# Kernel optimization log

Measured on AMD Instinct MI355X. Metric: run time of the kernel, lower is better.

The kernel has to match this reference:

```python
import jax, jax.numpy as jnp
import numpy as np

B, N, F, O = 8, 4096, 512, 512
D = F // 8  # fc1/fc2 projection dim = 64


def setup_inputs() -> dict:
    key = jax.random.key(0)
    ks = jax.random.split(key, 8)
    x = jax.random.normal(ks[0], (B, N, F), dtype=jnp.float32)
    mask = jax.random.randint(ks[1], (B, N), 0, 2).astype(jnp.float32)
    s1 = 1.0 / np.sqrt(F)
    w1 = jax.random.uniform(ks[2], (F, D), jnp.float32, -s1, s1)
    b1 = jnp.zeros((D,), jnp.float32)
    w2 = jax.random.uniform(ks[3], (F, D), jnp.float32, -s1, s1)
    b2 = jnp.zeros((D,), jnp.float32)
    s2 = 1.0 / np.sqrt(O)
    weight = jax.random.uniform(ks[4], (F, O), jnp.float32, -s2, s2)
    return {"x": x, "mask": mask, "w1": w1, "b1": b1, "w2": w2, "b2": b2, "weight": weight}


def reference(x, mask, w1, b1, w2, b2, weight):
    # q, k: [B, N, D]
    q = x @ w1 + b1
    k = x @ w2 + b2
    scale = jnp.sqrt(jnp.asarray(D, x.dtype))
    # sim: [B, N, N]
    sim = jnp.einsum('bnd,bmd->bnm', q, k) / scale
    # NOTE: mask.unsqueeze(-1) -> [B, N, 1]: masks QUERY rows (faithful to source)
    neg = jnp.asarray(-1e12, x.dtype)
    sim = sim + (1.0 - mask)[:, :, None] * neg
    adj = jax.nn.softmax(sim, axis=-1) * mask[:, :, None]
    support = x @ weight  # [B, N, O]
    return jnp.einsum('bnm,bmo->bno', adj, support)
```

## Files before the change

kernel.cpp:

```cpp
#include <hip/hip_runtime.h>

constexpr int BB = 8, NN = 4096, FF = 512, DD = 64, OO = 512;

using short8  = __attribute__((ext_vector_type(8))) short;
using ushort8 = __attribute__((ext_vector_type(8))) unsigned short;
using ushort4v= __attribute__((ext_vector_type(4))) unsigned short;
using f32x4   = __attribute__((ext_vector_type(4))) float;

__device__ __forceinline__ unsigned short f2bf(float f) {
  unsigned int u = __builtin_bit_cast(unsigned int, f);
  return (unsigned short)((u + 0x7FFFu + ((u >> 16) & 1u)) >> 16);
}

__device__ __forceinline__ f32x4 mfma16(short8 a, short8 b, f32x4 c) {
  return __builtin_amdgcn_mfma_f32_16x16x32_bf16(a, b, c, 0, 0, 0);
}

__device__ __forceinline__ void gl_lds16(const void* g, void* s) {
  __builtin_amdgcn_global_load_lds(
      (const __attribute__((address_space(1))) unsigned int*)g,
      (__attribute__((address_space(3))) unsigned int*)s,
      16, 0, 0);
}

__global__ void cast_x(const float* __restrict__ x, unsigned short* __restrict__ xb) {
  size_t base = ((size_t)blockIdx.x * 256 + threadIdx.x) * 8;
  float4 a = *(const float4*)(x + base);
  float4 b = *(const float4*)(x + base + 4);
  ushort8 o;
  o[0]=f2bf(a.x); o[1]=f2bf(a.y); o[2]=f2bf(a.z); o[3]=f2bf(a.w);
  o[4]=f2bf(b.x); o[5]=f2bf(b.y); o[6]=f2bf(b.z); o[7]=f2bf(b.w);
  *(ushort8*)(xb + base) = o;
}

__global__ void build_w(const float* __restrict__ w1, const float* __restrict__ w2,
                        const float* __restrict__ wgt,
                        const float* __restrict__ b1, const float* __restrict__ b2,
                        unsigned short* __restrict__ Wt, float* __restrict__ bias) {
  int idx = blockIdx.x * 256 + threadIdx.x;
  int j = idx >> 9, kk = idx & 511;
  float v = (j < 64) ? w1[kk * 64 + j]
          : (j < 128) ? w2[kk * 64 + (j - 64)]
                      : wgt[(size_t)kk * 512 + (j - 128)];
  Wt[(size_t)j * 512 + kk] = f2bf(v);
  if (kk == 0) bias[j] = (j < 64) ? b1[j] : (j < 128) ? b2[j - 64] : 0.f;
}

__global__ void compact_rows(const float* __restrict__ mask, int* __restrict__ cnt,
                             int* __restrict__ ridx) {
  __shared__ int wsum[4];
  __shared__ int base;
  const int b = blockIdx.x;
  const int t = threadIdx.x, lane = t & 63, w = t >> 6;
  if (t == 0) base = 0;
  __syncthreads();
  for (int it = 0; it < 16; ++it) {
    int r = it * 256 + t;
    bool act = mask[(b << 12) + r] != 0.f;
    unsigned long long bal = __ballot(act);
    int pre = __popcll(bal & ((1ull << lane) - 1ull));
    if (lane == 0) wsum[w] = __popcll(bal);
    __syncthreads();
    int woff = 0;
    for (int i = 0; i < w; ++i) woff += wsum[i];
    int tot = wsum[0] + wsum[1] + wsum[2] + wsum[3];
    if (act) ridx[(b << 12) + base + woff + pre] = r;
    __syncthreads();
    if (t == 0) base += tot;
    __syncthreads();
  }
  if (t == 0) cnt[b] = base;
}

__global__ void zero_masked(const float* __restrict__ mask, float* __restrict__ out) {
  int gid = blockIdx.x * 256 + threadIdx.x;
  int r = gid >> 7, c = (gid & 127) * 4;
  if (mask[r] == 0.f) {
    float4 z = {0.f, 0.f, 0.f, 0.f};
    *(float4*)(out + (size_t)r * 512 + c) = z;
  }
}

__global__ __launch_bounds__(256, 2) void proj_gemm(
    const unsigned short* __restrict__ X, const unsigned short* __restrict__ Wt,
    const float* __restrict__ bias,
    unsigned short* __restrict__ QK, unsigned short* __restrict__ SupT) {
  __shared__ __align__(16) unsigned short Abuf[128 * 64];
  __shared__ __align__(16) unsigned short Bbuf[128 * 64];
  const int t = threadIdx.x, lane = t & 63, w = t >> 6;
  const int nblk = blockIdx.x;
  const int m0 = blockIdx.y * 128, n0 = nblk * 128;
  const int wm = w & 1, wn = w >> 1;

  f32x4 acc[4][4] = {};
  for (int kt = 0; kt < 8; ++kt) {
    for (int i = 0; i < 4; ++i) {
      int c = i * 4 + w;
      int row = c * 8 + (lane >> 3);
      int k0 = (lane & 7) * 8;
      gl_lds16(X + (size_t)(m0 + row) * 512 + kt * 64 + k0, &Abuf[c * 512]);
      gl_lds16(Wt + (size_t)(n0 + row) * 512 + kt * 64 + k0, &Bbuf[c * 512]);
    }
    __syncthreads();
    short8 af[4][2], bfr[4][2];
    for (int mi = 0; mi < 4; ++mi)
      for (int kc = 0; kc < 2; ++kc) {
        int row = wm * 64 + mi * 16 + (lane & 15);
        int d = kc * 32 + (lane >> 4) * 8;
        af[mi][kc] = *(const short8*)&Abuf[row * 64 + d];
      }
    for (int ni = 0; ni < 4; ++ni)
      for (int kc = 0; kc < 2; ++kc) {
        int col = wn * 64 + ni * 16 + (lane & 15);
        int d = kc * 32 + (lane >> 4) * 8;
        bfr[ni][kc] = *(const short8*)&Bbuf[col * 64 + d];
      }
    for (int mi = 0; mi < 4; ++mi)
      for (int ni = 0; ni < 4; ++ni)
        for (int kc = 0; kc < 2; ++kc)
          acc[mi][ni] = mfma16(af[mi][kc], bfr[ni][kc], acc[mi][ni]);
    __syncthreads();
  }
  for (int mi = 0; mi < 4; ++mi)
    for (int ni = 0; ni < 4; ++ni) {
      int col_g = n0 + wn * 64 + ni * 16 + (lane & 15);
      int row0 = m0 + wm * 64 + mi * 16 + ((lane >> 4) * 4);
      float bv = bias[col_g];
      if (nblk == 0) {
        for (int j = 0; j < 4; ++j)
          QK[(size_t)(row0 + j) * 128 + col_g] = f2bf(acc[mi][ni][j] + bv);
      } else {
        int scol = col_g - 128;
        int b = row0 >> 12, rl = row0 & 4095;
        ushort4v pk;
        for (int j = 0; j < 4; ++j) pk[j] = f2bf(acc[mi][ni][j] + bv);
        *(ushort4v*)&SupT[(size_t)(b * 512 + scol) * 4096 + rl] = pk;
      }
    }
}

__global__ __launch_bounds__(512, 6) void attn_kernel(
    const unsigned short* __restrict__ QK, const unsigned short* __restrict__ SupT,
    const int* __restrict__ cnt, const int* __restrict__ ridx,
    float* __restrict__ out) {
  __shared__ __align__(16) unsigned short Kb[2][32 * 64];
  __shared__ __align__(16) unsigned short Vt[2][256 * 32];
  __shared__ __align__(16) unsigned short Pb[2][64 * 40];
  __shared__ float lsh[2][64];
  __shared__ int rsh[64];

  const int batch = blockIdx.x & 7;
  const int rest  = blockIdx.x >> 3;
  const int chunk = rest >> 1, colh = rest & 1;
  const int n_act = cnt[batch];
  if (chunk * 64 >= n_act) return;
  const int rem = min(64, n_act - chunk * 64);

  const int t = threadIdx.x, lane = t & 63, w = t >> 6;
  const int keybase = batch << 12;
  const int wm = w >> 2;
  const int wq = w & 3;
  const int fms = wq >> 1, ks = wq & 1;
  const int wo = w & 3;

  if (t < 64) rsh[t] = ridx[(batch << 12) + chunk * 64 + min(t, rem - 1)];
  __syncthreads();

  short8 aq[2];
  {
    int rl = rsh[wm * 32 + fms * 16 + (lane & 15)];
    for (int kc = 0; kc < 2; ++kc)
      aq[kc] = *(const short8*)&QK[(size_t)(keybase + rl) * 128 + kc * 32 + (lane >> 4) * 8];
  }

  f32x4 acc[2][4] = {};
  float lacc[4] = {0.f, 0.f, 0.f, 0.f};
  const int rl0 = wm * 32 + fms * 16 + (lane >> 4) * 4;

  auto stage = [&](int p, int key0) {
    if (w < 4) {
      int key = w * 8 + (lane >> 3);
      int q = lane & 7;
      int d0 = (q ^ (key & 7)) * 8;
      gl_lds16(QK + (size_t)(keybase + key0 + key) * 128 + 64 + d0, &Kb[p][w * 512]);
    }
    for (int i = 0; i < 2; ++i) {
      int c = i * 8 + w;
      int colL = c * 16 + (lane >> 2);
      int q = lane & 3;
      int k0 = (q ^ ((colL >> 1) & 3)) * 8;
      gl_lds16(SupT + (size_t)(batch * 512 + colh * 256 + colL) * 4096 + key0 + k0,
               &Vt[p][c * 512]);
    }
  };

  stage(0, 0);
  for (int kt = 0; kt < 128; ++kt) {
    const int p = kt & 1;
    asm volatile("s_waitcnt vmcnt(0)" ::: "memory");
    asm volatile("s_barrier" ::: "memory");

    if (kt < 127) stage(p ^ 1, (kt + 1) * 32);

    {
      f32x4 sa = {0.f, 0.f, 0.f, 0.f};
      int key = ks * 16 + (lane & 15);
      __builtin_amdgcn_s_setprio(1);
      for (int kc = 0; kc < 2; ++kc) {
        int dblk = kc * 4 + (lane >> 4);
        int blk = dblk ^ (key & 7);
        short8 bk = *(const short8*)&Kb[p][key * 64 + blk * 8];
        sa = mfma16(aq[kc], bk, sa);
      }
      __builtin_amdgcn_s_setprio(0);
      for (int j = 0; j < 4; ++j) {
        float pv = __expf(sa[j] * 0.125f);
        lacc[j] += pv;
        Pb[p][(rl0 + j) * 40 + key] = f2bf(pv);
      }
    }
    asm volatile("s_waitcnt lgkmcnt(0)" ::: "memory");
    asm volatile("s_barrier" ::: "memory");

    short8 pa[2];
    for (int fm = 0; fm < 2; ++fm) {
      int row = wm * 32 + fm * 16 + (lane & 15);
      pa[fm] = *(const short8*)&Pb[p][row * 40 + (lane >> 4) * 8];
    }
    __builtin_amdgcn_s_setprio(1);
    for (int ni = 0; ni < 4; ++ni) {
      int colL = wo * 64 + ni * 16 + (lane & 15);
      int blk = (lane >> 4) ^ ((colL >> 1) & 3);
      short8 vb = *(const short8*)&Vt[p][colL * 32 + blk * 8];
      acc[0][ni] = mfma16(pa[0], vb, acc[0][ni]);
      acc[1][ni] = mfma16(pa[1], vb, acc[1][ni]);
    }
    __builtin_amdgcn_s_setprio(0);
  }

  for (int j = 0; j < 4; ++j) {
    float v = lacc[j];
    v += __shfl_xor(v, 1); v += __shfl_xor(v, 2);
    v += __shfl_xor(v, 4); v += __shfl_xor(v, 8);
    lacc[j] = v;
  }
  if ((lane & 15) == 0) {
    for (int j = 0; j < 4; ++j) lsh[ks][rl0 + j] = lacc[j];
  }
  __syncthreads();

  for (int fm = 0; fm < 2; ++fm)
    for (int ni = 0; ni < 4; ++ni) {
      int colL = wo * 64 + ni * 16 + (lane & 15);
      int sl0 = wm * 32 + fm * 16 + (lane >> 4) * 4;
      for (int j = 0; j < 4; ++j) {
        if (sl0 + j < rem) {
          float linv = 1.f / (lsh[0][sl0 + j] + lsh[1][sl0 + j]);
          int rl = rsh[sl0 + j];
          float av = ((float*)&acc[fm][ni])[j];
          out[(size_t)(keybase + rl) * 512 + colh * 256 + colL] = av * linv;
        }
      }
    }
}

extern "C" void kernel_launch(void* const* d_in, const int* in_sizes, int n_in,
                              void* d_out, int out_size, void* d_ws, size_t ws_size,
                              hipStream_t stream) {
  const float* x    = (const float*)d_in[0];
  const float* mask = (const float*)d_in[1];
  const float* w1   = (const float*)d_in[2];
  const float* b1   = (const float*)d_in[3];
  const float* w2   = (const float*)d_in[4];
  const float* b2   = (const float*)d_in[5];
  const float* wgt  = (const float*)d_in[6];
  float* out = (float*)d_out;

  char* ws = (char*)d_ws;
  unsigned short* Xb   = (unsigned short*)(ws);
  unsigned short* QK   = (unsigned short*)(ws + 33554432);
  unsigned short* SupT = (unsigned short*)(ws + 41943040);
  unsigned short* Wt   = (unsigned short*)(ws + 75497472);
  float* bias          = (float*)(ws + 76152832);
  int*   cnt           = (int*)(ws + 76417536);
  int*   ridx          = (int*)(ws + 76417664);

  build_w<<<dim3(1280), dim3(256), 0, stream>>>(w1, w2, wgt, b1, b2, Wt, bias);
  compact_rows<<<dim3(8), dim3(256), 0, stream>>>(mask, cnt, ridx);
  cast_x<<<dim3(8192), dim3(256), 0, stream>>>(x, Xb);
  proj_gemm<<<dim3(5, 256), dim3(256), 0, stream>>>(Xb, Wt, bias, QK, SupT);
  attn_kernel<<<dim3(1024), dim3(512), 0, stream>>>(QK, SupT, cnt, ridx, out);
  zero_masked<<<dim3(16384), dim3(256), 0, stream>>>(mask, out);
}
```

Before: 233.0 us.

## Keep attention probabilities in registers via 32x32 MFMA and lane shuffles

Restructures the attention inner loop around 32x32x16 bf16 MFMAs. Each wave computes the transposed score tile S^T = K·Q^T for all 32 keys itself, so the exponentiated probabilities are packed with v_cvt_pk_bf16_f32 and rearranged by cross-half shuffles directly into the A operand of the P·V MFMA. This removes the LDS round trip for P and the second barrier per key tile. In exchange, the QK^T product is computed redundantly by the four column waves of each row group, register pressure rises, and the occupancy hint drops from 6 to 4.

```diff
diff --git a/kernel.cpp b/kernel.cpp
--- a/kernel.cpp
+++ b/kernel.cpp
@@ -5,7 +5,9 @@
 using short8  = __attribute__((ext_vector_type(8))) short;
 using ushort8 = __attribute__((ext_vector_type(8))) unsigned short;
 using ushort4v= __attribute__((ext_vector_type(4))) unsigned short;
+using uint4v  = __attribute__((ext_vector_type(4))) unsigned int;
 using f32x4   = __attribute__((ext_vector_type(4))) float;
+using f32x16  = __attribute__((ext_vector_type(16))) float;
 
 __device__ __forceinline__ unsigned short f2bf(float f) {
   unsigned int u = __builtin_bit_cast(unsigned int, f);
@@ -14,6 +16,9 @@
 
 __device__ __forceinline__ f32x4 mfma16(short8 a, short8 b, f32x4 c) {
   return __builtin_amdgcn_mfma_f32_16x16x32_bf16(a, b, c, 0, 0, 0);
+}
+__device__ __forceinline__ f32x16 mfma32(short8 a, short8 b, f32x16 c) {
+  return __builtin_amdgcn_mfma_f32_32x32x16_bf16(a, b, c, 0, 0, 0);
 }
 
 __device__ __forceinline__ void gl_lds16(const void* g, void* s) {
@@ -139,14 +144,13 @@
     }
 }
 
-__global__ __launch_bounds__(512, 6) void attn_kernel(
+__global__ __launch_bounds__(512, 4) void attn_kernel(
     const unsigned short* __restrict__ QK, const unsigned short* __restrict__ SupT,
     const int* __restrict__ cnt, const int* __restrict__ ridx,
     float* __restrict__ out) {
   __shared__ __align__(16) unsigned short Kb[2][32 * 64];
   __shared__ __align__(16) unsigned short Vt[2][256 * 32];
-  __shared__ __align__(16) unsigned short Pb[2][64 * 40];
-  __shared__ float lsh[2][64];
+  __shared__ float lsh2[2][32];
   __shared__ int rsh[64];
 
   const int batch = blockIdx.x & 7;
@@ -159,23 +163,24 @@
   const int t = threadIdx.x, lane = t & 63, w = t >> 6;
   const int keybase = batch << 12;
   const int wm = w >> 2;
-  const int wq = w & 3;
-  const int fms = wq >> 1, ks = wq & 1;
   const int wo = w & 3;
+  const int l31 = lane & 31, g = lane >> 5;
 
   if (t < 64) rsh[t] = ridx[(batch << 12) + chunk * 64 + min(t, rem - 1)];
   __syncthreads();
 
-  short8 aq[2];
+  short8 qf[4];
   {
-    int rl = rsh[wm * 32 + fms * 16 + (lane & 15)];
-    for (int kc = 0; kc < 2; ++kc)
-      aq[kc] = *(const short8*)&QK[(size_t)(keybase + rl) * 128 + kc * 32 + (lane >> 4) * 8];
-  }
-
-  f32x4 acc[2][4] = {};
-  float lacc[4] = {0.f, 0.f, 0.f, 0.f};
-  const int rl0 = wm * 32 + fms * 16 + (lane >> 4) * 4;
+    int rl = rsh[wm * 32 + l31];
+    const unsigned short* qp = QK + (size_t)(keybase + rl) * 128 + g * 8;
+    qf[0] = *(const short8*)(qp);
+    qf[1] = *(const short8*)(qp + 16);
+    qf[2] = *(const short8*)(qp + 32);
+    qf[3] = *(const short8*)(qp + 48);
+  }
+
+  f32x16 accA = {}, accB = {};
+  float lacc = 0.f;
 
   auto stage = [&](int p, int key0) {
     if (w < 4) {
@@ -199,69 +204,70 @@
     const int p = kt & 1;
     asm volatile("s_waitcnt vmcnt(0)" ::: "memory");
     asm volatile("s_barrier" ::: "memory");
-
     if (kt < 127) stage(p ^ 1, (kt + 1) * 32);
 
+    f32x16 st = {};
+    __builtin_amdgcn_s_setprio(1);
+#pragma unroll
+    for (int d = 0; d < 4; ++d) {
+      short8 kf = *(const short8*)&Kb[p][l31 * 64 + (((d << 1) + g) ^ (l31 & 7)) * 8];
+      st = mfma32(kf, qf[d], st);
+    }
+    __builtin_amdgcn_s_setprio(0);
+
+    float pv[16];
+#pragma unroll
+    for (int r = 0; r < 16; ++r) { pv[r] = __expf(st[r] * 0.125f); lacc += pv[r]; }
+    unsigned wpk[8];
+#pragma unroll
+    for (int i = 0; i < 8; ++i) {
+      unsigned u;
+      asm("v_cvt_pk_bf16_f32 %0, %1, %2" : "=v"(u) : "v"(pv[2 * i]), "v"(pv[2 * i + 1]));
+      wpk[i] = u;
+    }
+    unsigned r0 = (unsigned)__shfl_xor((int)(g ? wpk[0] : wpk[2]), 32);
+    unsigned r1 = (unsigned)__shfl_xor((int)(g ? wpk[1] : wpk[3]), 32);
+    unsigned r2 = (unsigned)__shfl_xor((int)(g ? wpk[4] : wpk[6]), 32);
+    unsigned r3 = (unsigned)__shfl_xor((int)(g ? wpk[5] : wpk[7]), 32);
+    uint4v a0v = g ? (uint4v){r0, r1, wpk[2], wpk[3]} : (uint4v){wpk[0], wpk[1], r0, r1};
+    uint4v a1v = g ? (uint4v){r2, r3, wpk[6], wpk[7]} : (uint4v){wpk[4], wpk[5], r2, r3};
+    short8 pa0 = __builtin_bit_cast(short8, a0v);
+    short8 pa1 = __builtin_bit_cast(short8, a1v);
+
     {
-      f32x4 sa = {0.f, 0.f, 0.f, 0.f};
-      int key = ks * 16 + (lane & 15);
+      int colL = wo * 64 + l31;
+      int sw = (colL >> 1) & 3;
+      const unsigned short* vb0 = &Vt[p][colL * 32];
+      const unsigned short* vb1 = vb0 + 32 * 32;
+      short8 v00 = *(const short8*)(vb0 + ((g ^ sw) << 3));
+      short8 v01 = *(const short8*)(vb0 + (((2 + g) ^ sw) << 3));
+      short8 v10 = *(const short8*)(vb1 + ((g ^ sw) << 3));
+      short8 v11 = *(const short8*)(vb1 + (((2 + g) ^ sw) << 3));
       __builtin_amdgcn_s_setprio(1);
-      for (int kc = 0; kc < 2; ++kc) {
-        int dblk = kc * 4 + (lane >> 4);
-        int blk = dblk ^ (key & 7);
-        short8 bk = *(const short8*)&Kb[p][key * 64 + blk * 8];
-        sa = mfma16(aq[kc], bk, sa);
-      }
+      accA = mfma32(pa0, v00, accA);
+      accA = mfma32(pa1, v01, accA);
+      accB = mfma32(pa0, v10, accB);
+      accB = mfma32(pa1, v11, accB);
       __builtin_amdgcn_s_setprio(0);
-      for (int j = 0; j < 4; ++j) {
-        float pv = __expf(sa[j] * 0.125f);
-        lacc[j] += pv;
-        Pb[p][(rl0 + j) * 40 + key] = f2bf(pv);
-      }
-    }
-    asm volatile("s_waitcnt lgkmcnt(0)" ::: "memory");
-    asm volatile("s_barrier" ::: "memory");
-
-    short8 pa[2];
-    for (int fm = 0; fm < 2; ++fm) {
-      int row = wm * 32 + fm * 16 + (lane & 15);
-      pa[fm] = *(const short8*)&Pb[p][row * 40 + (lane >> 4) * 8];
-    }
-    __builtin_amdgcn_s_setprio(1);
-    for (int ni = 0; ni < 4; ++ni) {
-      int colL = wo * 64 + ni * 16 + (lane & 15);
-      int blk = (lane >> 4) ^ ((colL >> 1) & 3);
-      short8 vb = *(const short8*)&Vt[p][colL * 32 + blk * 8];
-      acc[0][ni] = mfma16(pa[0], vb, acc[0][ni]);
-      acc[1][ni] = mfma16(pa[1], vb, acc[1][ni]);
-    }
-    __builtin_amdgcn_s_setprio(0);
-  }
-
-  for (int j = 0; j < 4; ++j) {
-    float v = lacc[j];
-    v += __shfl_xor(v, 1); v += __shfl_xor(v, 2);
-    v += __shfl_xor(v, 4); v += __shfl_xor(v, 8);
-    lacc[j] = v;
-  }
-  if ((lane & 15) == 0) {
-    for (int j = 0; j < 4; ++j) lsh[ks][rl0 + j] = lacc[j];
-  }
+    }
+  }
+
+  float ltot = lacc + __shfl_xor(lacc, 32);
+  if (wo == 0 && lane < 32) lsh2[wm][lane] = 1.f / ltot;
   __syncthreads();
 
-  for (int fm = 0; fm < 2; ++fm)
-    for (int ni = 0; ni < 4; ++ni) {
-      int colL = wo * 64 + ni * 16 + (lane & 15);
-      int sl0 = wm * 32 + fm * 16 + (lane >> 4) * 4;
-      for (int j = 0; j < 4; ++j) {
-        if (sl0 + j < rem) {
-          float linv = 1.f / (lsh[0][sl0 + j] + lsh[1][sl0 + j]);
-          int rl = rsh[sl0 + j];
-          float av = ((float*)&acc[fm][ni])[j];
-          out[(size_t)(keybase + rl) * 512 + colh * 256 + colL] = av * linv;
-        }
-      }
-    }
+#pragma unroll
+  for (int reg = 0; reg < 16; ++reg) {
+    int qrow = (reg & 3) + 8 * (reg >> 2) + 4 * g;
+    int slot = wm * 32 + qrow;
+    if (slot < rem) {
+      float linv = lsh2[wm][qrow];
+      int rl = rsh[slot];
+      float* op = out + (size_t)(keybase + rl) * 512 + colh * 256 + wo * 64 + l31;
+      op[0]  = accA[reg] * linv;
+      op[32] = accB[reg] * linv;
+    }
+  }
 }
 
 extern "C" void kernel_launch(void* const* d_in, const int* in_sizes, int n_in,
```

New measurement: 334.3 us. +43.5%, slower.

## Shrink attention blocks to 32 query rows and 128 output columns

Applied to the files above, without the earlier changes.

The attention kernel now runs 4096 blocks of 256 threads, each covering 32 compacted query rows and a quarter of the output columns, instead of 1024 blocks of 512 threads covering 64 rows and half the columns. The QK^T MFMA is transposed so each lane produces keys for one row, which shrinks the row-sum reduction to two shuffles. The bf16 pack now uses v_cvt_pk_bf16_f32 with a single 8-byte store into LDS. The smaller grid cells are meant to balance load across CUs given a variable active-row count, but each block now reloads the K tiles for fewer rows and columns, which raises total K/V traffic.

```diff
diff --git a/kernel.cpp b/kernel.cpp
--- a/kernel.cpp
+++ b/kernel.cpp
@@ -139,57 +139,56 @@
     }
 }
 
-__global__ __launch_bounds__(512, 6) void attn_kernel(
+__global__ __launch_bounds__(256, 4) void attn_kernel(
     const unsigned short* __restrict__ QK, const unsigned short* __restrict__ SupT,
     const int* __restrict__ cnt, const int* __restrict__ ridx,
     float* __restrict__ out) {
   __shared__ __align__(16) unsigned short Kb[2][32 * 64];
-  __shared__ __align__(16) unsigned short Vt[2][256 * 32];
-  __shared__ __align__(16) unsigned short Pb[2][64 * 40];
-  __shared__ float lsh[2][64];
-  __shared__ int rsh[64];
+  __shared__ __align__(16) unsigned short Vt[2][128 * 32];
+  __shared__ __align__(16) unsigned short Pb[2][32 * 40];
+  __shared__ float lsh[2][32];
+  __shared__ int rsh[32];
 
   const int batch = blockIdx.x & 7;
   const int rest  = blockIdx.x >> 3;
-  const int chunk = rest >> 1, colh = rest & 1;
+  const int chunk = rest >> 2, colq = rest & 3;
   const int n_act = cnt[batch];
-  if (chunk * 64 >= n_act) return;
-  const int rem = min(64, n_act - chunk * 64);
+  if (chunk * 32 >= n_act) return;
+  const int rem = min(32, n_act - chunk * 32);
 
   const int t = threadIdx.x, lane = t & 63, w = t >> 6;
   const int keybase = batch << 12;
-  const int wm = w >> 2;
-  const int wq = w & 3;
-  const int fms = wq >> 1, ks = wq & 1;
-  const int wo = w & 3;
-
-  if (t < 64) rsh[t] = ridx[(batch << 12) + chunk * 64 + min(t, rem - 1)];
+  const int l15 = lane & 15, lh = lane >> 4;
+  const int rg = w >> 1, ks = w & 1;
+  const int wo = w;
+
+  if (t < 32) rsh[t] = ridx[(batch << 12) + chunk * 32 + min(t, rem - 1)];
   __syncthreads();
 
   short8 aq[2];
   {
-    int rl = rsh[wm * 32 + fms * 16 + (lane & 15)];
-    for (int kc = 0; kc < 2; ++kc)
-      aq[kc] = *(const short8*)&QK[(size_t)(keybase + rl) * 128 + kc * 32 + (lane >> 4) * 8];
-  }
-
-  f32x4 acc[2][4] = {};
-  float lacc[4] = {0.f, 0.f, 0.f, 0.f};
-  const int rl0 = wm * 32 + fms * 16 + (lane >> 4) * 4;
+    int rl = rsh[rg * 16 + l15];
+    const unsigned short* qp = QK + (size_t)(keybase + rl) * 128 + lh * 8;
+    aq[0] = *(const short8*)(qp);
+    aq[1] = *(const short8*)(qp + 32);
+  }
+
+  f32x4 acc[2][2] = {};
+  float lacc = 0.f;
 
   auto stage = [&](int p, int key0) {
-    if (w < 4) {
+    {
       int key = w * 8 + (lane >> 3);
       int q = lane & 7;
       int d0 = (q ^ (key & 7)) * 8;
       gl_lds16(QK + (size_t)(keybase + key0 + key) * 128 + 64 + d0, &Kb[p][w * 512]);
     }
     for (int i = 0; i < 2; ++i) {
-      int c = i * 8 + w;
+      int c = i * 4 + w;
       int colL = c * 16 + (lane >> 2);
       int q = lane & 3;
       int k0 = (q ^ ((colL >> 1) & 3)) * 8;
-      gl_lds16(SupT + (size_t)(batch * 512 + colh * 256 + colL) * 4096 + key0 + k0,
+      gl_lds16(SupT + (size_t)(batch * 512 + colq * 128 + colL) * 4096 + key0 + k0,
                &Vt[p][c * 512]);
     }
   };
@@ -198,67 +197,62 @@
   for (int kt = 0; kt < 128; ++kt) {
     const int p = kt & 1;
     asm volatile("s_waitcnt vmcnt(0)" ::: "memory");
-    asm volatile("s_barrier" ::: "memory");
-
+    __builtin_amdgcn_s_barrier();
     if (kt < 127) stage(p ^ 1, (kt + 1) * 32);
 
+    f32x4 st = {};
+    __builtin_amdgcn_s_setprio(1);
+#pragma unroll
+    for (int kc = 0; kc < 2; ++kc) {
+      int key = ks * 16 + l15;
+      int blk = (kc * 4 + lh) ^ (key & 7);
+      short8 kf = *(const short8*)&Kb[p][key * 64 + blk * 8];
+      st = mfma16(kf, aq[kc], st);
+    }
+    __builtin_amdgcn_s_setprio(0);
+
     {
-      f32x4 sa = {0.f, 0.f, 0.f, 0.f};
-      int key = ks * 16 + (lane & 15);
-      __builtin_amdgcn_s_setprio(1);
-      for (int kc = 0; kc < 2; ++kc) {
-        int dblk = kc * 4 + (lane >> 4);
-        int blk = dblk ^ (key & 7);
-        short8 bk = *(const short8*)&Kb[p][key * 64 + blk * 8];
-        sa = mfma16(aq[kc], bk, sa);
-      }
-      __builtin_amdgcn_s_setprio(0);
-      for (int j = 0; j < 4; ++j) {
-        float pv = __expf(sa[j] * 0.125f);
-        lacc[j] += pv;
-        Pb[p][(rl0 + j) * 40 + key] = f2bf(pv);
-      }
+      float e0 = __expf(st[0] * 0.125f), e1 = __expf(st[1] * 0.125f);
+      float e2 = __expf(st[2] * 0.125f), e3 = __expf(st[3] * 0.125f);
+      lacc += (e0 + e1) + (e2 + e3);
+      unsigned u0, u1;
+      asm("v_cvt_pk_bf16_f32 %0, %1, %2" : "=v"(u0) : "v"(e0), "v"(e1));
+      asm("v_cvt_pk_bf16_f32 %0, %1, %2" : "=v"(u1) : "v"(e2), "v"(e3));
+      uint2 pk; pk.x = u0; pk.y = u1;
+      *(uint2*)&Pb[p][(rg * 16 + l15) * 40 + ks * 16 + lh * 4] = pk;
     }
     asm volatile("s_waitcnt lgkmcnt(0)" ::: "memory");
-    asm volatile("s_barrier" ::: "memory");
-
-    short8 pa[2];
-    for (int fm = 0; fm < 2; ++fm) {
-      int row = wm * 32 + fm * 16 + (lane & 15);
-      pa[fm] = *(const short8*)&Pb[p][row * 40 + (lane >> 4) * 8];
-    }
+    __builtin_amdgcn_s_barrier();
+
+    short8 pa0 = *(const short8*)&Pb[p][l15 * 40 + lh * 8];
+    short8 pa1 = *(const short8*)&Pb[p][(16 + l15) * 40 + lh * 8];
     __builtin_amdgcn_s_setprio(1);
-    for (int ni = 0; ni < 4; ++ni) {
-      int colL = wo * 64 + ni * 16 + (lane & 15);
-      int blk = (lane >> 4) ^ ((colL >> 1) & 3);
+#pragma unroll
+    for (int ni = 0; ni < 2; ++ni) {
+      int colL = wo * 32 + ni * 16 + l15;
+      int blk = lh ^ ((colL >> 1) & 3);
       short8 vb = *(const short8*)&Vt[p][colL * 32 + blk * 8];
-      acc[0][ni] = mfma16(pa[0], vb, acc[0][ni]);
-      acc[1][ni] = mfma16(pa[1], vb, acc[1][ni]);
+      acc[0][ni] = mfma16(pa0, vb, acc[0][ni]);
+      acc[1][ni] = mfma16(pa1, vb, acc[1][ni]);
     }
     __builtin_amdgcn_s_setprio(0);
   }
 
-  for (int j = 0; j < 4; ++j) {
-    float v = lacc[j];
-    v += __shfl_xor(v, 1); v += __shfl_xor(v, 2);
-    v += __shfl_xor(v, 4); v += __shfl_xor(v, 8);
-    lacc[j] = v;
-  }
-  if ((lane & 15) == 0) {
-    for (int j = 0; j < 4; ++j) lsh[ks][rl0 + j] = lacc[j];
-  }
+  lacc += __shfl_xor(lacc, 16);
+  lacc += __shfl_xor(lacc, 32);
+  if (lh == 0) lsh[ks][rg * 16 + l15] = lacc;
   __syncthreads();
 
   for (int fm = 0; fm < 2; ++fm)
-    for (int ni = 0; ni < 4; ++ni) {
-      int colL = wo * 64 + ni * 16 + (lane & 15);
-      int sl0 = wm * 32 + fm * 16 + (lane >> 4) * 4;
+    for (int ni = 0; ni < 2; ++ni) {
+      int colL = wo * 32 + ni * 16 + l15;
+      int sl0 = fm * 16 + lh * 4;
       for (int j = 0; j < 4; ++j) {
         if (sl0 + j < rem) {
           float linv = 1.f / (lsh[0][sl0 + j] + lsh[1][sl0 + j]);
           int rl = rsh[sl0 + j];
           float av = ((float*)&acc[fm][ni])[j];
-          out[(size_t)(keybase + rl) * 512 + colh * 256 + colL] = av * linv;
+          out[(size_t)(keybase + rl) * 512 + colq * 128 + colL] = av * linv;
         }
       }
     }
@@ -289,6 +283,6 @@
   compact_rows<<<dim3(8), dim3(256), 0, stream>>>(mask, cnt, ridx);
   cast_x<<<dim3(8192), dim3(256), 0, stream>>>(x, Xb);
   proj_gemm<<<dim3(5, 256), dim3(256), 0, stream>>>(Xb, Wt, bias, QK, SupT);
-  attn_kernel<<<dim3(1024), dim3(512), 0, stream>>>(QK, SupT, cnt, ridx, out);
+  attn_kernel<<<dim3(4096), dim3(256), 0, stream>>>(QK, SupT, cnt, ridx, out);
   zero_masked<<<dim3(16384), dim3(256), 0, stream>>>(mask, out);
 }
```

New measurement: 301.9 us. 29.6% more time.

## Split attention key range across two blocks with atomic accumulation and separate normalization

Applied to the files above, without the earlier changes.

Splits the key dimension of the attention kernel into two halves handled by separate blocks, doubling the grid to 2048 blocks. Each block accumulates unnormalized outputs and softmax row sums into global memory with atomicAdd. A pre-zero kernel clears the output and the row-sum buffer, and a new normalize pass divides each active row by its sum, replacing the masked-row zeroing. This is meant to raise parallelism and occupancy, at the cost of atomic traffic, an extra full read-modify-write pass over the output, and nondeterministic summation order.

```diff
diff --git a/kernel.cpp b/kernel.cpp
--- a/kernel.cpp
+++ b/kernel.cpp
@@ -72,13 +72,26 @@
   if (t == 0) cnt[b] = base;
 }
 
-__global__ void zero_masked(const float* __restrict__ mask, float* __restrict__ out) {
+__global__ void zero_out(float* __restrict__ out, float* __restrict__ lbuf) {
   int gid = blockIdx.x * 256 + threadIdx.x;
-  int r = gid >> 7, c = (gid & 127) * 4;
-  if (mask[r] == 0.f) {
-    float4 z = {0.f, 0.f, 0.f, 0.f};
-    *(float4*)(out + (size_t)r * 512 + c) = z;
-  }
+  float4 z = {0.f, 0.f, 0.f, 0.f};
+  *(float4*)(out + (size_t)gid * 4) = z;
+  if (gid < 8192) *(float4*)(lbuf + gid * 4) = z;
+}
+
+__global__ void normalize_rows(const float* __restrict__ lbuf, const int* __restrict__ cnt,
+                               const int* __restrict__ ridx, float* __restrict__ out) {
+  int gid = blockIdx.x * 256 + threadIdx.x;
+  int b = gid >> 19;
+  int rest = gid & ((1 << 19) - 1);
+  int slot = rest >> 7, c4 = (rest & 127) * 4;
+  if (slot >= cnt[b]) return;
+  int row = ridx[(b << 12) + slot];
+  float linv = 1.f / lbuf[(b << 12) + slot];
+  float* p = out + ((size_t)(b * 4096 + row)) * 512 + c4;
+  float4 v = *(float4*)p;
+  v.x *= linv; v.y *= linv; v.z *= linv; v.w *= linv;
+  *(float4*)p = v;
 }
 
 __global__ __launch_bounds__(256, 2) void proj_gemm(
@@ -139,10 +152,10 @@
     }
 }
 
-__global__ __launch_bounds__(512, 6) void attn_kernel(
+__global__ __launch_bounds__(512, 3) void attn_kernel(
     const unsigned short* __restrict__ QK, const unsigned short* __restrict__ SupT,
     const int* __restrict__ cnt, const int* __restrict__ ridx,
-    float* __restrict__ out) {
+    float* __restrict__ lbuf, float* __restrict__ out) {
   __shared__ __align__(16) unsigned short Kb[2][32 * 64];
   __shared__ __align__(16) unsigned short Vt[2][256 * 32];
   __shared__ __align__(16) unsigned short Pb[2][64 * 40];
@@ -151,13 +164,16 @@
 
   const int batch = blockIdx.x & 7;
   const int rest  = blockIdx.x >> 3;
-  const int chunk = rest >> 1, colh = rest & 1;
+  const int chunk = rest >> 2;
+  const int colh  = (rest >> 1) & 1;
+  const int kh    = rest & 1;
   const int n_act = cnt[batch];
   if (chunk * 64 >= n_act) return;
   const int rem = min(64, n_act - chunk * 64);
 
   const int t = threadIdx.x, lane = t & 63, w = t >> 6;
   const int keybase = batch << 12;
+  const int khbase = kh * 2048;
   const int wm = w >> 2;
   const int wq = w & 3;
   const int fms = wq >> 1, ks = wq & 1;
@@ -174,7 +190,7 @@
   }
 
   f32x4 acc[2][4] = {};
-  float lacc[4] = {0.f, 0.f, 0.f, 0.f};
+  float lacc = 0.f;
   const int rl0 = wm * 32 + fms * 16 + (lane >> 4) * 4;
 
   auto stage = [&](int p, int key0) {
@@ -194,13 +210,12 @@
     }
   };
 
-  stage(0, 0);
-  for (int kt = 0; kt < 128; ++kt) {
+  stage(0, khbase);
+  for (int kt = 0; kt < 64; ++kt) {
     const int p = kt & 1;
     asm volatile("s_waitcnt vmcnt(0)" ::: "memory");
-    asm volatile("s_barrier" ::: "memory");
-
-    if (kt < 127) stage(p ^ 1, (kt + 1) * 32);
+    __builtin_amdgcn_s_barrier();
+    if (kt < 63) stage(p ^ 1, khbase + (kt + 1) * 32);
 
     {
       f32x4 sa = {0.f, 0.f, 0.f, 0.f};
@@ -215,12 +230,12 @@
       __builtin_amdgcn_s_setprio(0);
       for (int j = 0; j < 4; ++j) {
         float pv = __expf(sa[j] * 0.125f);
-        lacc[j] += pv;
+        lacc += pv;
         Pb[p][(rl0 + j) * 40 + key] = f2bf(pv);
       }
     }
     asm volatile("s_waitcnt lgkmcnt(0)" ::: "memory");
-    asm volatile("s_barrier" ::: "memory");
+    __builtin_amdgcn_s_barrier();
 
     short8 pa[2];
     for (int fm = 0; fm < 2; ++fm) {
@@ -238,14 +253,9 @@
     __builtin_amdgcn_s_setprio(0);
   }
 
-  for (int j = 0; j < 4; ++j) {
-    float v = lacc[j];
-    v += __shfl_xor(v, 1); v += __shfl_xor(v, 2);
-    v += __shfl_xor(v, 4); v += __shfl_xor(v, 8);
-    lacc[j] = v;
-  }
-  if ((lane & 15) == 0) {
-    for (int j = 0; j < 4; ++j) lsh[ks][rl0 + j] = lacc[j];
+  {
+    float v = lacc;
+    (void)v;
   }
   __syncthreads();
 
@@ -255,10 +265,143 @@
       int sl0 = wm * 32 + fm * 16 + (lane >> 4) * 4;
       for (int j = 0; j < 4; ++j) {
         if (sl0 + j < rem) {
-          float linv = 1.f / (lsh[0][sl0 + j] + lsh[1][sl0 + j]);
           int rl = rsh[sl0 + j];
-          float av = ((float*)&acc[fm][ni])[j];
-          out[(size_t)(keybase + rl) * 512 + colh * 256 + colL] = av * linv;
+          atomicAdd(out + (size_t)(keybase + rl) * 512 + colh * 256 + colL,
+                    ((float*)&acc[fm][ni])[j]);
+        }
+      }
+    }
+  (void)lsh;
+}
+
+
+extern "C" void kernel_launch(void* const* d_in, const int* in_sizes, int n_in,
+                              void* d_out, int out_size, void* d_ws, size_t ws_size,
+                              hipStream_t stream);
+
+__global__ __launch_bounds__(512, 3) void attn_kernel2(
+    const unsigned short* __restrict__ QK, const unsigned short* __restrict__ SupT,
+    const int* __restrict__ cnt, const int* __restrict__ ridx,
+    float* __restrict__ lbuf, float* __restrict__ out) {
+  __shared__ __align__(16) unsigned short Kb[2][32 * 64];
+  __shared__ __align__(16) unsigned short Vt[2][256 * 32];
+  __shared__ __align__(16) unsigned short Pb[2][64 * 40];
+  __shared__ float lsh[2][64];
+  __shared__ int rsh[64];
+
+  const int batch = blockIdx.x & 7;
+  const int rest  = blockIdx.x >> 3;
+  const int chunk = rest >> 2;
+  const int colh  = (rest >> 1) & 1;
+  const int kh    = rest & 1;
+  const int n_act = cnt[batch];
+  if (chunk * 64 >= n_act) return;
+  const int rem = min(64, n_act - chunk * 64);
+
+  const int t = threadIdx.x, lane = t & 63, w = t >> 6;
+  const int keybase = batch << 12;
+  const int khbase = kh * 2048;
+  const int wm = w >> 2;
+  const int wq = w & 3;
+  const int fms = wq >> 1, ks = wq & 1;
+  const int wo = w & 3;
+
+  if (t < 64) rsh[t] = ridx[(batch << 12) + chunk * 64 + min(t, rem - 1)];
+  __syncthreads();
+
+  short8 aq[2];
+  {
+    int rl = rsh[wm * 32 + fms * 16 + (lane & 15)];
+    for (int kc = 0; kc < 2; ++kc)
+      aq[kc] = *(const short8*)&QK[(size_t)(keybase + rl) * 128 + kc * 32 + (lane >> 4) * 8];
+  }
+
+  f32x4 acc[2][4] = {};
+  float lacc4[4] = {0.f, 0.f, 0.f, 0.f};
+  const int rl0 = wm * 32 + fms * 16 + (lane >> 4) * 4;
+
+  auto stage = [&](int p, int key0) {
+    if (w < 4) {
+      int key = w * 8 + (lane >> 3);
+      int q = lane & 7;
+      int d0 = (q ^ (key & 7)) * 8;
+      gl_lds16(QK + (size_t)(keybase + key0 + key) * 128 + 64 + d0, &Kb[p][w * 512]);
+    }
+    for (int i = 0; i < 2; ++i) {
+      int c = i * 8 + w;
+      int colL = c * 16 + (lane >> 2);
+      int q = lane & 3;
+      int k0 = (q ^ ((colL >> 1) & 3)) * 8;
+      gl_lds16(SupT + (size_t)(batch * 512 + colh * 256 + colL) * 4096 + key0 + k0,
+               &Vt[p][c * 512]);
+    }
+  };
+
+  stage(0, khbase);
+  for (int kt = 0; kt < 64; ++kt) {
+    const int p = kt & 1;
+    asm volatile("s_waitcnt vmcnt(0)" ::: "memory");
+    __builtin_amdgcn_s_barrier();
+    if (kt < 63) stage(p ^ 1, khbase + (kt + 1) * 32);
+
+    {
+      f32x4 sa = {0.f, 0.f, 0.f, 0.f};
+      int key = ks * 16 + (lane & 15);
+      __builtin_amdgcn_s_setprio(1);
+      for (int kc = 0; kc < 2; ++kc) {
+        int dblk = kc * 4 + (lane >> 4);
+        int blk = dblk ^ (key & 7);
+        short8 bk = *(const short8*)&Kb[p][key * 64 + blk * 8];
+        sa = mfma16(aq[kc], bk, sa);
+      }
+      __builtin_amdgcn_s_setprio(0);
+      for (int j = 0; j < 4; ++j) {
+        float pv = __expf(sa[j] * 0.125f);
+        lacc4[j] += pv;
+        Pb[p][(rl0 + j) * 40 + key] = f2bf(pv);
+      }
+    }
+    asm volatile("s_waitcnt lgkmcnt(0)" ::: "memory");
+    __builtin_amdgcn_s_barrier();
+
+    short8 pa[2];
+    for (int fm = 0; fm < 2; ++fm) {
+      int row = wm * 32 + fm * 16 + (lane & 15);
+      pa[fm] = *(const short8*)&Pb[p][row * 40 + (lane >> 4) * 8];
+    }
+    __builtin_amdgcn_s_setprio(1);
+    for (int ni = 0; ni < 4; ++ni) {
+      int colL = wo * 64 + ni * 16 + (lane & 15);
+      int blk = (lane >> 4) ^ ((colL >> 1) & 3);
+      short8 vb = *(const short8*)&Vt[p][colL * 32 + blk * 8];
+      acc[0][ni] = mfma16(pa[0], vb, acc[0][ni]);
+      acc[1][ni] = mfma16(pa[1], vb, acc[1][ni]);
+    }
+    __builtin_amdgcn_s_setprio(0);
+  }
+
+  for (int j = 0; j < 4; ++j) {
+    float v = lacc4[j];
+    v += __shfl_xor(v, 1); v += __shfl_xor(v, 2);
+    v += __shfl_xor(v, 4); v += __shfl_xor(v, 8);
+    lacc4[j] = v;
+  }
+  if ((lane & 15) == 0)
+    for (int j = 0; j < 4; ++j) lsh[ks][rl0 + j] = lacc4[j];
+  __syncthreads();
+
+  if (colh == 0 && t < 64 && t < rem)
+    atomicAdd(&lbuf[(batch << 12) + chunk * 64 + t], lsh[0][t] + lsh[1][t]);
+
+  for (int fm = 0; fm < 2; ++fm)
+    for (int ni = 0; ni < 4; ++ni) {
+      int colL = wo * 64 + ni * 16 + (lane & 15);
+      int sl0 = wm * 32 + fm * 16 + (lane >> 4) * 4;
+      for (int j = 0; j < 4; ++j) {
+        if (sl0 + j < rem) {
+          int rl = rsh[sl0 + j];
+          atomicAdd(out + (size_t)(keybase + rl) * 512 + colh * 256 + colL,
+                    ((float*)&acc[fm][ni])[j]);
         }
       }
     }
@@ -284,11 +427,13 @@
   float* bias          = (float*)(ws + 76152832);
   int*   cnt           = (int*)(ws + 76417536);
   int*   ridx          = (int*)(ws + 76417664);
+  float* lbuf          = (float*)(ws + 76548736);
 
   build_w<<<dim3(1280), dim3(256), 0, stream>>>(w1, w2, wgt, b1, b2, Wt, bias);
   compact_rows<<<dim3(8), dim3(256), 0, stream>>>(mask, cnt, ridx);
+  zero_out<<<dim3(16384), dim3(256), 0, stream>>>(out, lbuf);
   cast_x<<<dim3(8192), dim3(256), 0, stream>>>(x, Xb);
   proj_gemm<<<dim3(5, 256), dim3(256), 0, stream>>>(Xb, Wt, bias, QK, SupT);
-  attn_kernel<<<dim3(1024), dim3(512), 0, stream>>>(QK, SupT, cnt, ridx, out);
-  zero_masked<<<dim3(16384), dim3(256), 0, stream>>>(mask, out);
-}
+  attn_kernel2<<<dim3(2048), dim3(512), 0, stream>>>(QK, SupT, cnt, ridx, lbuf, out);
+  normalize_rows<<<dim3(16384), dim3(256), 0, stream>>>(lbuf, cnt, ridx, out);
+}
```

New measurement: 256.4 us. 10.1% more time.
